# Kernel optimization log

Hardware: AMD Instinct MI355X
Metric: run time of the kernel (lower is better)

The kernel has to match this reference:

```python
import jax, jax.numpy as jnp
import numpy as np

IN, OUT, WS = 128, 64, 512
B, H, W = 4, 128, 128
GAIN = (2.0 / (1.0 + 0.2 ** 2)) ** 0.5  # util.lrelu_gain for leaky_relu(0.2)
EPS = 1e-8


def up2_bilinear_ac(x):
    # bilinear upsample x2, align_corners=True (torch F.upsample_bilinear semantics)
    _, _, h, w = x.shape
    ys = jnp.linspace(0.0, h - 1.0, 2 * h)
    xs = jnp.linspace(0.0, w - 1.0, 2 * w)
    y0 = jnp.floor(ys).astype(jnp.int32)
    y1 = jnp.minimum(y0 + 1, h - 1)
    wy = (ys - y0).astype(x.dtype)
    x0 = jnp.floor(xs).astype(jnp.int32)
    x1 = jnp.minimum(x0 + 1, w - 1)
    wx = (xs - x0).astype(x.dtype)
    t = x[:, :, y0, :] * (1 - wy)[None, None, :, None] + x[:, :, y1, :] * wy[None, None, :, None]
    return t[:, :, :, x0] * (1 - wx) + t[:, :, :, x1] * wx


def convt3(x, w):
    # torch conv_transpose2d(stride=1, padding=1, k=3) == conv2d with spatially
    # flipped kernel, weight layout [I,O,3,3] -> lax 'IOHW' spec, SAME padding.
    wf = w[:, :, ::-1, ::-1]
    return jax.lax.conv_general_dilated(
        x, wf, (1, 1), ((1, 1), (1, 1)),
        dimension_numbers=('NCHW', 'IOHW', 'NCHW'))


def mod_conv(x, style, w, he):
    # StyleGAN2 modulate + demodulate, expressed in fused activation form:
    # y[b,o] = demod[b,o] * convT(x[b] * style[b,:,None,None], he*W)  (same math
    # as building the per-sample grouped weight tensor in the original).
    wh = w * he                                  # [I,O,3,3]
    wsq = jnp.sum(wh * wh, axis=(2, 3))          # [I,O]
    d = jax.lax.rsqrt(jnp.einsum('bi,io->bo', style * style, wsq) + EPS)  # [B,O]
    y = convt3(x * style[:, :, None, None], wh)
    return y * d[:, :, None, None] * GAIN        # forward also multiplies by gain


def setup_inputs() -> dict:
    key = jax.random.key(0)
    ks = jax.random.split(key, 16)
    f = lambda k, s: jax.random.normal(k, s, dtype=jnp.float32)
    return {
        'x': f(ks[0], (B, IN, H, W)),
        'w': f(ks[1], (B, WS, 1, 1)),
        'conv1_w': f(ks[2], (IN, OUT, 3, 3)),
        'conv2_w': f(ks[3], (OUT, OUT, 3, 3)),
        'bias1': jnp.zeros((1, OUT, 1, 1), jnp.float32),
        'bias2': jnp.zeros((1, OUT, 1, 1), jnp.float32),
        'aaff1_w': f(ks[4], (IN, WS)),
        'aaff1_b': jnp.zeros((IN,), jnp.float32),
        'aaff2_w': f(ks[5], (OUT, WS)),
        'aaff2_b': jnp.zeros((OUT,), jnp.float32),
        'baff1_w': f(ks[6], (OUT,)) * 0.1,
        'baff2_w': f(ks[7], (OUT,)) * 0.1,
        'rgb_w': f(ks[8], (3, OUT)),
        'rgb_b': jnp.zeros((3,), jnp.float32),
        'noise1': f(ks[9], (B, 1, 2 * H, 2 * W)),
        'noise2': f(ks[10], (B, 1, 2 * H, 2 * W)),
    }


def reference(x, w, conv1_w, conv2_w, bias1, bias2, aaff1_w, aaff1_b,
              aaff2_w, aaff2_b, baff1_w, baff2_w, rgb_w, rgb_b,
              noise1, noise2):
    he1 = GAIN / (IN * 9) ** 0.5
    he2 = GAIN / (OUT * 9) ** 0.5
    he_a = 1.0 / WS ** 0.5
    he_rgb = 0.03 / OUT ** 0.5

    xu = up2_bilinear_ac(x)                       # [B,IN,2H,2W]
    wv = w[:, :, 0, 0]                            # [B,WS]

    s1 = jnp.einsum('ow,bw->bo', aaff1_w * he_a, wv) + aaff1_b
    h = mod_conv(xu, s1, conv1_w, he1)
    h = h + noise1 * baff1_w[None, :, None, None] + bias1
    h = jax.nn.leaky_relu(h, 0.2)

    s2 = jnp.einsum('ow,bw->bo', aaff2_w * he_a, wv) + aaff2_b
    h = mod_conv(h, s2, conv2_w, he2)
    h = h + noise2 * baff2_w[None, :, None, None] + bias2
    h = jax.nn.leaky_relu(h, 0.2)

    rgb = jnp.einsum('oc,bchw->bohw', rgb_w * he_rgb, h) + rgb_b[None, :, None, None]
    return (h, rgb)
```

## Files before the change

### kernel.cpp

```cpp
#include <hip/hip_runtime.h>
#include <hip/hip_bf16.h>
#include <math.h>

#define BN 4
#define CIN 128
#define COUT 64
#define WSDIM 512
#define HI 128
#define WI 128
#define HO 256
#define WO 256
#define EPSC 1e-8f
#define GAINC 1.3867504905630728f
#define HE1 (GAINC/33.941125496954285f)
#define HE2 (GAINC/24.0f)
#define SUP (127.0f/255.0f)

typedef __attribute__((ext_vector_type(8))) short s16x8;
typedef __attribute__((ext_vector_type(4))) float f32x4_t;
typedef __attribute__((ext_vector_type(4))) unsigned int u32x4;

static __device__ __forceinline__ float lrelu(float v){ return v > 0.f ? v : 0.2f*v; }
static __device__ __forceinline__ unsigned short bfbits(float v){
  __hip_bfloat16 h = __float2bfloat16(v);
  return *reinterpret_cast<unsigned short*>(&h);
}
static __device__ __forceinline__ unsigned int packbf(float a, float b){
  return (unsigned int)bfbits(a) | ((unsigned int)bfbits(b) << 16);
}
static __device__ __forceinline__ void gload_lds16(const void* g, void* l){
  __builtin_amdgcn_global_load_lds(
      (const __attribute__((address_space(1))) void*)g,
      (__attribute__((address_space(3))) void*)l, 16, 0, 0);
}

__global__ __launch_bounds__(256) void k_prep(
    const float* __restrict__ w, const float* __restrict__ c1w, const float* __restrict__ c2w,
    const float* __restrict__ a1w, const float* __restrict__ a1b,
    const float* __restrict__ a2w, const float* __restrict__ a2b,
    unsigned short* __restrict__ B1, unsigned short* __restrict__ B2,
    float* __restrict__ s1, float* __restrict__ s2,
    float* __restrict__ d1g, float* __restrict__ d2g,
    unsigned int* __restrict__ zpage)
{
  const int g = blockIdx.x, t = threadIdx.x;
  __shared__ float sh1[CIN];
  __shared__ float sh2[COUT];
  if (g < 144) {
    if (g == 0 && t < 64) zpage[t] = 0u;
    int cc = g / 36, r = g - cc * 36, k = r >> 2, ot = r & 3;
    for (int e = t; e < 512; e += 256) {
      int l = e >> 3, j = e & 7;
      int c = cc * 32 + (l >> 4) * 8 + j, o = ot * 16 + (l & 15);
      B1[g * 512 + e] = bfbits(c1w[(c * COUT + o) * 9 + (8 - k)] * HE1);
    }
  } else if (g < 288) {
    int g2 = g - 144;
    int cc = g2 / 36, r = g2 - cc * 36, k = r >> 2, ot = r & 3;
    for (int e = t; e < 512; e += 256) {
      int l = e >> 3, j = e & 7;
      int c = cc * 32 + (l >> 4) * 8 + j, o = ot * 16 + (l & 15);
      B2[g2 * 512 + e] = bfbits(c2w[(c * COUT + o) * 9 + (8 - k)] * HE2);
    }
  } else {
    const int b = g - 288;
    const float he_a = 0.044194173824159216f;
    const float* wv = w + b * WSDIM;
    if (t < CIN) {
      float acc = 0.f;
      const float* ap = a1w + t * WSDIM;
      for (int k = 0; k < WSDIM; ++k) acc += ap[k] * wv[k];
      float v = acc * he_a + a1b[t];
      sh1[t] = v; s1[b * CIN + t] = v;
    } else if (t < CIN + COUT) {
      int o = t - CIN;
      float acc = 0.f;
      const float* ap = a2w + o * WSDIM;
      for (int k = 0; k < WSDIM; ++k) acc += ap[k] * wv[k];
      float v = acc * he_a + a2b[o];
      sh2[o] = v; s2[b * COUT + o] = v;
    }
    __syncthreads();
    const int o = t >> 2, p = t & 3;
    float acc = 0.f;
    for (int c = p * 32; c < p * 32 + 32; ++c) {
      const float* wp = c1w + (size_t)(c * COUT + o) * 9;
      float ws_ = 0.f;
      #pragma unroll
      for (int k = 0; k < 9; ++k) ws_ += wp[k] * wp[k];
      acc += sh1[c] * sh1[c] * ws_;
    }
    acc += __shfl_xor(acc, 1); acc += __shfl_xor(acc, 2);
    if (p == 0) d1g[b * COUT + o] = rsqrtf(acc * HE1 * HE1 + EPSC) * GAINC;
    float ac2 = 0.f;
    for (int c = p * 16; c < p * 16 + 16; ++c) {
      const float* wp = c2w + (size_t)(c * COUT + o) * 9;
      float ws_ = 0.f;
      #pragma unroll
      for (int k = 0; k < 9; ++k) ws_ += wp[k] * wp[k];
      ac2 += sh2[c] * sh2[c] * ws_;
    }
    ac2 += __shfl_xor(ac2, 1); ac2 += __shfl_xor(ac2, 2);
    if (p == 0) d2g[b * COUT + o] = rsqrtf(ac2 * HE2 * HE2 + EPSC) * GAINC;
  }
}

__global__ __launch_bounds__(256) void k_conv1(
    const float* __restrict__ x, const unsigned short* __restrict__ B1pre,
    const float* __restrict__ s1, const float* __restrict__ noise1,
    const float* __restrict__ bias1, const float* __restrict__ baff1,
    const float* __restrict__ d1g, const float* __restrict__ s2,
    unsigned short* __restrict__ h1)
{
  const int id = blockIdx.x;
  const int swz = (id & 7) * 256 + (id >> 3);
  const int b = swz >> 9;
  const int oy0 = ((swz >> 4) & 31) * 8, ox0 = (swz & 15) * 16;
  const int tid = threadIdx.x;
  const int lane = tid & 63, wv = tid >> 6;
  const int lx = lane & 15, lg = lane >> 4;

  __shared__ __align__(16) float patch[3584];
  __shared__ __align__(16) unsigned int ldsA[180 * 16];
  __shared__ float s1L[CIN];

  const int ty = oy0 > 0 ? oy0 - 1 : 0;
  const int tx = ox0 > 0 ? ox0 - 1 : 0;
  const int py0 = min((ty * 127) / 255, HI - 7);
  const int px0 = min((tx * 127) / 255, WI - 12);
  const int px0a = px0 & ~3;

  if (tid < CIN) s1L[tid] = s1[b * CIN + tid];

  f32x4_t acc[2][4];
  #pragma unroll
  for (int i = 0; i < 2; ++i)
    #pragma unroll
    for (int j = 0; j < 4; ++j) acc[i][j] = (f32x4_t){0.f, 0.f, 0.f, 0.f};

  auto STAGE = [&](int cc) {
    const float* xb = x + (((size_t)b * CIN + cc * 32) << 14);
    #pragma unroll
    for (int i = 0; i < 3; ++i) {
      int ub = i * 256 + (wv << 6);
      int u = ub + lane;
      int p_ = u / 28, rem = u - p_ * 28;
      int ch = ((p_ & 3) << 3) | (p_ >> 2);
      int rr = rem >> 2, ck = rem & 3;
      int col = min(px0a + ck * 4, 124);
      const float* src = xb + ((size_t)ch << 14) + (py0 + rr) * WI + col;
      gload_lds16((const void*)src, (void*)&patch[(size_t)ub * 4]);
    }
    if (wv < 2) {
      int ub = 768 + (wv << 6);
      int u = ub + lane;
      int p_ = u / 28, rem = u - p_ * 28;
      int ch = ((p_ & 3) << 3) | (p_ >> 2);
      int rr = rem >> 2, ck = rem & 3;
      int col = min(px0a + ck * 4, 124);
      const float* src = xb + ((size_t)ch << 14) + (py0 + rr) * WI + col;
      gload_lds16((const void*)src, (void*)&patch[(size_t)ub * 4]);
    }
  };

  const s16x8* Bb = (const s16x8*)B1pre;

  STAGE(0);
  __syncthreads();
  for (int cc = 0; cc < 4; ++cc) {
    for (int e = tid; e < 720; e += 256) {
      int pos = e >> 2, q = e & 3;
      int ys = pos / 18, xs = pos - ys * 18;
      int yy = oy0 - 1 + ys, xx = ox0 - 1 + xs;
      u32x4 outv = {0u, 0u, 0u, 0u};
      if (yy >= 0 && yy < HO && xx >= 0 && xx < WO) {
        float fy = yy * SUP; int y0 = (int)fy; float wy = fy - (float)y0;
        float fx = xx * SUP; int x0 = (int)fx; float wx = fx - (float)x0;
        int r0 = y0 - py0, r1 = min(y0 + 1, HI - 1) - py0;
        int c0 = x0 - px0a;
        float v[8];
        #pragma unroll
        for (int j = 0; j < 8; ++j) {
          const float* pc = &patch[(j * 4 + q) * 112];
          float tl = pc[r0 * 16 + c0], tr = pc[r0 * 16 + c0 + 1];
          float bl = pc[r1 * 16 + c0], br = pc[r1 * 16 + c0 + 1];
          float t0 = tl + (bl - tl) * wy;
          float t1 = tr + (br - tr) * wy;
          v[j] = (t0 + (t1 - t0) * wx) * s1L[cc * 32 + q * 8 + j];
        }
        outv = (u32x4){packbf(v[0], v[1]), packbf(v[2], v[3]),
                       packbf(v[4], v[5]), packbf(v[6], v[7])};
      }
      *(u32x4*)(ldsA + pos * 16 + q * 4) = outv;
    }
    __syncthreads();
    if (cc < 3) STAGE(cc + 1);
    #pragma unroll
    for (int k = 0; k < 9; ++k) {
      const int dy = k / 3, dx = k - 3 * (k / 3);
      s16x8 b0 = Bb[((cc * 9 + k) * 4 + 0) * 64 + lane];
      s16x8 b1 = Bb[((cc * 9 + k) * 4 + 1) * 64 + lane];
      s16x8 b2 = Bb[((cc * 9 + k) * 4 + 2) * 64 + lane];
      s16x8 b3 = Bb[((cc * 9 + k) * 4 + 3) * 64 + lane];
      #pragma unroll
      for (int yi = 0; yi < 2; ++yi) {
        int row = (wv * 2 + yi + dy) * 18 + (lx + dx);
        s16x8 a = *(const s16x8*)((const char*)ldsA + (size_t)row * 64 + lg * 16);
        acc[yi][0] = __builtin_amdgcn_mfma_f32_16x16x32_bf16(a, b0, acc[yi][0], 0, 0, 0);
        acc[yi][1] = __builtin_amdgcn_mfma_f32_16x16x32_bf16(a, b1, acc[yi][1], 0, 0, 0);
        acc[yi][2] = __builtin_amdgcn_mfma_f32_16x16x32_bf16(a, b2, acc[yi][2], 0, 0, 0);
        acc[yi][3] = __builtin_amdgcn_mfma_f32_16x16x32_bf16(a, b3, acc[yi][3], 0, 0, 0);
      }
    }
    if (cc < 3) __syncthreads();
  }
  #pragma unroll
  for (int yi = 0; yi < 2; ++yi) {
    int y = oy0 + wv * 2 + yi;
    f32x4_t nv = *(const f32x4_t*)(noise1 + (size_t)b * HO * WO + (size_t)y * WO + ox0 + lg * 4);
    #pragma unroll
    for (int ot = 0; ot < 4; ++ot) {
      int o = ot * 16 + lx;
      float d = d1g[b * COUT + o], ba = baff1[o], bi = bias1[o], sv = s2[b * COUT + o];
      #pragma unroll
      for (int jj = 0; jj < 4; ++jj) {
        float v = acc[yi][ot][jj] * d + nv[jj] * ba + bi;
        v = lrelu(v) * sv;
        int xg = ox0 + lg * 4 + jj;
        h1[(((size_t)b * HO + y) * WO + xg) * COUT + o] = bfbits(v);
      }
    }
  }
}

__global__ __launch_bounds__(256) void k_conv2(
    const unsigned short* __restrict__ h1, const unsigned short* __restrict__ B2pre,
    const float* __restrict__ noise2, const float* __restrict__ bias2, const float* __restrict__ baff2,
    const float* __restrict__ d2g, const float* __restrict__ rgbw, const float* __restrict__ rgbb,
    const unsigned int* __restrict__ zpage,
    float* __restrict__ hout, float* __restrict__ rgbout)
{
  const int id = blockIdx.x;
  const int swz = (id & 7) * 128 + (id >> 3);
  const int b = swz >> 8;
  const int oy0 = ((swz >> 4) & 15) * 16, ox0 = (swz & 15) * 16;
  const int tid = threadIdx.x;
  const int lane = tid & 63, wv = tid >> 6;
  const int lx = lane & 15, lg = lane >> 4;

  __shared__ __align__(16) unsigned int ldsA[2][1536 * 4];

  f32x4_t acc[4][4];
  #pragma unroll
  for (int i = 0; i < 4; ++i)
    #pragma unroll
    for (int j = 0; j < 4; ++j) acc[i][j] = (f32x4_t){0.f, 0.f, 0.f, 0.f};

  const s16x8* Bb = (const s16x8*)B2pre;

  const int e0u = __builtin_amdgcn_readfirstlane(tid & ~63);
  #pragma unroll
  for (int cc = 0; cc < 2; ++cc) {
    #pragma unroll
    for (int i = 0; i < 6; ++i) {
      int ebase = i * 256 + e0u;
      int e = ebase + lane;
      int pos = e >> 2, q = e & 3;
      int ys = pos / 18, xs = pos - ys * 18;
      int yy = oy0 - 1 + ys, xx = ox0 - 1 + xs;
      bool ok = (e < 1296) && (yy >= 0) && (yy < HO) && (xx >= 0) && (xx < WO);
      const void* src = ok
          ? (const void*)(h1 + ((((size_t)b * HO + yy) * WO + xx) * COUT) + cc * 32 + q * 8)
          : (const void*)zpage;
      gload_lds16(src, (void*)&ldsA[cc][(size_t)ebase * 4]);
    }
  }
  __syncthreads();

  #pragma unroll
  for (int cc = 0; cc < 2; ++cc) {
    const char* bufc = (const char*)ldsA[cc];
    #pragma unroll
    for (int k = 0; k < 9; ++k) {
      const int dy = k / 3, dx = k - 3 * (k / 3);
      s16x8 b0 = Bb[((cc * 9 + k) * 4 + 0) * 64 + lane];
      s16x8 b1 = Bb[((cc * 9 + k) * 4 + 1) * 64 + lane];
      s16x8 b2 = Bb[((cc * 9 + k) * 4 + 2) * 64 + lane];
      s16x8 b3 = Bb[((cc * 9 + k) * 4 + 3) * 64 + lane];
      #pragma unroll
      for (int yi = 0; yi < 4; ++yi) {
        int row = (wv * 4 + yi + dy) * 18 + (lx + dx);
        s16x8 a = *(const s16x8*)(bufc + (size_t)row * 64 + lg * 16);
        acc[yi][0] = __builtin_amdgcn_mfma_f32_16x16x32_bf16(a, b0, acc[yi][0], 0, 0, 0);
        acc[yi][1] = __builtin_amdgcn_mfma_f32_16x16x32_bf16(a, b1, acc[yi][1], 0, 0, 0);
        acc[yi][2] = __builtin_amdgcn_mfma_f32_16x16x32_bf16(a, b2, acc[yi][2], 0, 0, 0);
        acc[yi][3] = __builtin_amdgcn_mfma_f32_16x16x32_bf16(a, b3, acc[yi][3], 0, 0, 0);
      }
    }
  }
  const float her = 0.03f / 8.0f;
  #pragma unroll
  for (int yi = 0; yi < 4; ++yi) {
    int y = oy0 + wv * 4 + yi;
    f32x4_t nv = *(const f32x4_t*)(noise2 + (size_t)b * HO * WO + (size_t)y * WO + ox0 + lg * 4);
    float r[3][4];
    #pragma unroll
    for (int ch = 0; ch < 3; ++ch)
      #pragma unroll
      for (int jj = 0; jj < 4; ++jj) r[ch][jj] = 0.f;
    #pragma unroll
    for (int ot = 0; ot < 4; ++ot) {
      int o = ot * 16 + lx;
      float d = d2g[b * COUT + o], ba = baff2[o], bi = bias2[o];
      float w0 = rgbw[o], w1 = rgbw[COUT + o], w2 = rgbw[2 * COUT + o];
      f32x4_t hv;
      #pragma unroll
      for (int jj = 0; jj < 4; ++jj) {
        float v = acc[yi][ot][jj] * d + nv[jj] * ba + bi;
        v = lrelu(v);
        hv[jj] = v;
        r[0][jj] += w0 * v; r[1][jj] += w1 * v; r[2][jj] += w2 * v;
      }
      *(f32x4_t*)(hout + ((size_t)(b * COUT + o) * HO + y) * WO + ox0 + lg * 4) = hv;
    }
    #pragma unroll
    for (int ch = 0; ch < 3; ++ch)
      #pragma unroll
      for (int jj = 0; jj < 4; ++jj) {
        float s = r[ch][jj];
        s += __shfl_xor(s, 1); s += __shfl_xor(s, 2);
        s += __shfl_xor(s, 4); s += __shfl_xor(s, 8);
        r[ch][jj] = s;
      }
    if (lx < 12) {
      float val = 0.f;
      #pragma unroll
      for (int ii = 0; ii < 12; ++ii) if (lx == ii) val = r[ii >> 2][ii & 3];
      int ch = lx >> 2, jj = lx & 3;
      rgbout[(((size_t)(b * 3 + ch)) * HO + y) * WO + ox0 + lg * 4 + jj] = val * her + rgbb[ch];
    }
  }
}

extern "C" void kernel_launch(void* const* d_in, const int* in_sizes, int n_in,
                              void* d_out, int out_size, void* d_ws, size_t ws_size,
                              hipStream_t stream) {
  const float* x      = (const float*)d_in[0];
  const float* w      = (const float*)d_in[1];
  const float* c1w    = (const float*)d_in[2];
  const float* c2w    = (const float*)d_in[3];
  const float* bias1  = (const float*)d_in[4];
  const float* bias2  = (const float*)d_in[5];
  const float* a1w    = (const float*)d_in[6];
  const float* a1b    = (const float*)d_in[7];
  const float* a2w    = (const float*)d_in[8];
  const float* a2b    = (const float*)d_in[9];
  const float* baff1  = (const float*)d_in[10];
  const float* baff2  = (const float*)d_in[11];
  const float* rgbw   = (const float*)d_in[12];
  const float* rgbb   = (const float*)d_in[13];
  const float* noise1 = (const float*)d_in[14];
  const float* noise2 = (const float*)d_in[15];

  const size_t h1_bytes = (size_t)BN * HO * WO * COUT * 2;
  unsigned short* h1 = (unsigned short*)d_ws;
  char* p = (char*)d_ws + h1_bytes;
  float* s1  = (float*)p;               p += BN * CIN * 4;
  float* s2  = (float*)p;               p += BN * COUT * 4;
  float* d1g = (float*)p;               p += BN * COUT * 4;
  float* d2g = (float*)p;               p += BN * COUT * 4;
  unsigned short* B1pre = (unsigned short*)p;  p += 144 * 512 * 2;
  unsigned short* B2pre = (unsigned short*)p;  p += 144 * 512 * 2;
  unsigned int* zpage = (unsigned int*)p;

  float* hout   = (float*)d_out;
  float* rgbout = hout + (size_t)BN * COUT * HO * WO;

  k_prep<<<292, 256, 0, stream>>>(w, c1w, c2w, a1w, a1b, a2w, a2b, B1pre, B2pre, s1, s2, d1g, d2g, zpage);
  k_conv1<<<2048, 256, 0, stream>>>(x, B1pre, s1, noise1, bias1, baff1, d1g, s2, h1);
  k_conv2<<<1024, 256, 0, stream>>>(h1, B2pre, noise2, bias2, baff2, d2g, rgbw, rgbb, zpage, hout, rgbout);
}
```

Baseline: 138.9 us.

## Pretranspose style-scaled input to channel-last bf16 before conv1

Adds a kernel that multiplies the input by the style vector, converts it to bf16 and transposes it to a channel-last layout. conv1 then stages the whole 7x13 pixel patch for all 128 channels once, instead of restaging an fp32 patch per 32-channel chunk. The bilinear gather reads 16-byte vectors of 8 packed channels and reuses precomputed interpolation indices. The cost is an extra kernel launch and an extra intermediate write and read of the input in global memory. The per-chunk prefetch overlap is removed, and the upsample input is now rounded to bf16 before interpolation rather than after.

```diff
diff --git a/kernel.cpp b/kernel.cpp
--- a/kernel.cpp
+++ b/kernel.cpp
@@ -105,10 +105,53 @@
   }
 }
 
+__global__ __launch_bounds__(256) void k_xt(
+    const float* __restrict__ x, const float* __restrict__ s1, unsigned short* __restrict__ XT)
+{
+  const int bid = blockIdx.x;
+  const int b = bid >> 7, y = bid & 127;
+  const int tid = threadIdx.x;
+  __shared__ float xs[32][133];
+  __shared__ float s1L[CIN];
+  if (tid < CIN) s1L[tid] = s1[b * CIN + tid];
+  const float* xb = x + (((size_t)b * CIN) << 14) + y * WI;
+  unsigned short* out = XT + (((size_t)(b * 128 + y)) << 7) * 128;
+
+  for (int chunk = 0; chunk < 4; ++chunk) {
+    __syncthreads();
+    {
+      int c = tid >> 3, x8 = (tid & 7) << 4;
+      const float* src = xb + (((size_t)(chunk * 32 + c)) << 14) + x8;
+      #pragma unroll
+      for (int k2 = 0; k2 < 4; ++k2) {
+        f32x4_t v = *(const f32x4_t*)(src + k2 * 4);
+        xs[c][x8 + k2 * 4 + 0] = v[0];
+        xs[c][x8 + k2 * 4 + 1] = v[1];
+        xs[c][x8 + k2 * 4 + 2] = v[2];
+        xs[c][x8 + k2 * 4 + 3] = v[3];
+      }
+    }
+    __syncthreads();
+    {
+      int xp = tid >> 1, half = tid & 1;
+      unsigned int pk[8];
+      #pragma unroll
+      for (int i2 = 0; i2 < 8; ++i2) {
+        int ch = half * 16 + i2 * 2;
+        float a  = xs[ch][xp]     * s1L[chunk * 32 + ch];
+        float bq = xs[ch + 1][xp] * s1L[chunk * 32 + ch + 1];
+        pk[i2] = packbf(a, bq);
+      }
+      unsigned short* dst = out + (size_t)xp * 128 + chunk * 32 + half * 16;
+      *(u32x4*)dst = *(u32x4*)pk;
+      *(u32x4*)(dst + 8) = *(u32x4*)(pk + 4);
+    }
+  }
+}
+
 __global__ __launch_bounds__(256) void k_conv1(
-    const float* __restrict__ x, const unsigned short* __restrict__ B1pre,
-    const float* __restrict__ s1, const float* __restrict__ noise1,
-    const float* __restrict__ bias1, const float* __restrict__ baff1,
+    const unsigned short* __restrict__ XT, const unsigned short* __restrict__ B1pre,
+    const float* __restrict__ noise1, const float* __restrict__ bias1, const float* __restrict__ baff1,
     const float* __restrict__ d1g, const float* __restrict__ s2,
     unsigned short* __restrict__ h1)
 {
@@ -120,81 +163,93 @@
   const int lane = tid & 63, wv = tid >> 6;
   const int lx = lane & 15, lg = lane >> 4;
 
-  __shared__ __align__(16) float patch[3584];
+  __shared__ __align__(16) unsigned int patch[1457 * 4];
   __shared__ __align__(16) unsigned int ldsA[180 * 16];
-  __shared__ float s1L[CIN];
 
   const int ty = oy0 > 0 ? oy0 - 1 : 0;
   const int tx = ox0 > 0 ? ox0 - 1 : 0;
   const int py0 = min((ty * 127) / 255, HI - 7);
-  const int px0 = min((tx * 127) / 255, WI - 12);
-  const int px0a = px0 & ~3;
-
-  if (tid < CIN) s1L[tid] = s1[b * CIN + tid];
-
-  f32x4_t acc[2][4];
-  #pragma unroll
-  for (int i = 0; i < 2; ++i)
-    #pragma unroll
-    for (int j = 0; j < 4; ++j) acc[i][j] = (f32x4_t){0.f, 0.f, 0.f, 0.f};
-
-  auto STAGE = [&](int cc) {
-    const float* xb = x + (((size_t)b * CIN + cc * 32) << 14);
-    #pragma unroll
-    for (int i = 0; i < 3; ++i) {
-      int ub = i * 256 + (wv << 6);
-      int u = ub + lane;
-      int p_ = u / 28, rem = u - p_ * 28;
-      int ch = ((p_ & 3) << 3) | (p_ >> 2);
-      int rr = rem >> 2, ck = rem & 3;
-      int col = min(px0a + ck * 4, 124);
-      const float* src = xb + ((size_t)ch << 14) + (py0 + rr) * WI + col;
-      gload_lds16((const void*)src, (void*)&patch[(size_t)ub * 4]);
-    }
-    if (wv < 2) {
-      int ub = 768 + (wv << 6);
-      int u = ub + lane;
-      int p_ = u / 28, rem = u - p_ * 28;
-      int ch = ((p_ & 3) << 3) | (p_ >> 2);
-      int rr = rem >> 2, ck = rem & 3;
-      int col = min(px0a + ck * 4, 124);
-      const float* src = xb + ((size_t)ch << 14) + (py0 + rr) * WI + col;
-      gload_lds16((const void*)src, (void*)&patch[(size_t)ub * 4]);
-    }
-  };
-
-  const s16x8* Bb = (const s16x8*)B1pre;
-
-  STAGE(0);
-  __syncthreads();
-  for (int cc = 0; cc < 4; ++cc) {
-    for (int e = tid; e < 720; e += 256) {
-      int pos = e >> 2, q = e & 3;
+  const int px0 = min((tx * 127) / 255, WI - 13);
+  const int q = tid & 3;
+
+  int a0[3], a1[3];
+  float gwy[3], gwx[3];
+  bool gok[3];
+  #pragma unroll
+  for (int i = 0; i < 3; ++i) {
+    int e = tid + i * 256;
+    gok[i] = false; a0[i] = 0; a1[i] = 0; gwy[i] = 0.f; gwx[i] = 0.f;
+    if (e < 720) {
+      int pos = e >> 2;
       int ys = pos / 18, xs = pos - ys * 18;
       int yy = oy0 - 1 + ys, xx = ox0 - 1 + xs;
-      u32x4 outv = {0u, 0u, 0u, 0u};
       if (yy >= 0 && yy < HO && xx >= 0 && xx < WO) {
-        float fy = yy * SUP; int y0 = (int)fy; float wy = fy - (float)y0;
-        float fx = xx * SUP; int x0 = (int)fx; float wx = fx - (float)x0;
+        gok[i] = true;
+        float fy = yy * SUP; int y0 = (int)fy; gwy[i] = fy - (float)y0;
+        float fx = xx * SUP; int x0 = (int)fx; gwx[i] = fx - (float)x0;
         int r0 = y0 - py0, r1 = min(y0 + 1, HI - 1) - py0;
-        int c0 = x0 - px0a;
-        float v[8];
-        #pragma unroll
-        for (int j = 0; j < 8; ++j) {
-          const float* pc = &patch[(j * 4 + q) * 112];
-          float tl = pc[r0 * 16 + c0], tr = pc[r0 * 16 + c0 + 1];
-          float bl = pc[r1 * 16 + c0], br = pc[r1 * 16 + c0 + 1];
-          float t0 = tl + (bl - tl) * wy;
-          float t1 = tr + (br - tr) * wy;
-          v[j] = (t0 + (t1 - t0) * wx) * s1L[cc * 32 + q * 8 + j];
+        int c0 = x0 - px0;
+        a0[i] = r0 * 13 + c0;
+        a1[i] = r1 * 13 + c0;
+      }
+    }
+  }
+
+  f32x4_t acc[2][4];
+  #pragma unroll
+  for (int i = 0; i < 2; ++i)
+    #pragma unroll
+    for (int j = 0; j < 4; ++j) acc[i][j] = (f32x4_t){0.f, 0.f, 0.f, 0.f};
+
+  if (tid == 0) { u32x4 z = {0u,0u,0u,0u}; *(u32x4*)(patch + (1456 << 2)) = z; }
+  #pragma unroll
+  for (int i = 0; i < 6; ++i) {
+    int u = tid + i * 256;
+    if (u < 1456) {
+      int g8 = u / 91, rem = u - g8 * 91;
+      int r = rem / 13, c = rem - r * 13;
+      const unsigned short* src = XT + ((((size_t)(b * 128 + py0 + r)) << 7) + (px0 + c)) * 128 + g8 * 8;
+      gload_lds16((const void*)src, (void*)(patch + ((size_t)u << 2)));
+    }
+  }
+  __syncthreads();
+
+  const s16x8* Bb = (const s16x8*)B1pre;
+  const u32x4* P = (const u32x4*)patch;
+
+  for (int cc = 0; cc < 4; ++cc) {
+    #pragma unroll
+    for (int i = 0; i < 3; ++i) {
+      int e = tid + i * 256;
+      if (e < 720) {
+        u32x4 outv = {0u, 0u, 0u, 0u};
+        if (gok[i]) {
+          int base = (cc * 4 + q) * 91;
+          u32x4 TL = P[base + a0[i]];
+          u32x4 TR = P[base + a0[i] + 1];
+          u32x4 BL = P[base + a1[i]];
+          u32x4 BR = P[base + a1[i] + 1];
+          float wy = gwy[i], wx = gwx[i];
+          #pragma unroll
+          for (int k2 = 0; k2 < 4; ++k2) {
+            float tl0 = __uint_as_float(TL[k2] << 16), tl1 = __uint_as_float(TL[k2] & 0xFFFF0000u);
+            float tr0 = __uint_as_float(TR[k2] << 16), tr1 = __uint_as_float(TR[k2] & 0xFFFF0000u);
+            float bl0 = __uint_as_float(BL[k2] << 16), bl1 = __uint_as_float(BL[k2] & 0xFFFF0000u);
+            float br0 = __uint_as_float(BR[k2] << 16), br1 = __uint_as_float(BR[k2] & 0xFFFF0000u);
+            float t0 = tl0 + (bl0 - tl0) * wy;
+            float t1 = tr0 + (br0 - tr0) * wy;
+            float v0 = t0 + (t1 - t0) * wx;
+            float u0 = tl1 + (bl1 - tl1) * wy;
+            float u1 = tr1 + (br1 - tr1) * wy;
+            float v1 = u0 + (u1 - u0) * wx;
+            outv[k2] = packbf(v0, v1);
+          }
         }
-        outv = (u32x4){packbf(v[0], v[1]), packbf(v[2], v[3]),
-                       packbf(v[4], v[5]), packbf(v[6], v[7])};
-      }
-      *(u32x4*)(ldsA + pos * 16 + q * 4) = outv;
+        int pos = (tid >> 2) + i * 64;
+        *(u32x4*)(ldsA + pos * 16 + q * 4) = outv;
+      }
     }
     __syncthreads();
-    if (cc < 3) STAGE(cc + 1);
     #pragma unroll
     for (int k = 0; k < 9; ++k) {
       const int dy = k / 3, dx = k - 3 * (k / 3);
@@ -371,12 +426,14 @@
   float* d2g = (float*)p;               p += BN * COUT * 4;
   unsigned short* B1pre = (unsigned short*)p;  p += 144 * 512 * 2;
   unsigned short* B2pre = (unsigned short*)p;  p += 144 * 512 * 2;
-  unsigned int* zpage = (unsigned int*)p;
+  unsigned int* zpage = (unsigned int*)p;      p += 256 * 4;
+  unsigned short* XT = (unsigned short*)p;
 
   float* hout   = (float*)d_out;
   float* rgbout = hout + (size_t)BN * COUT * HO * WO;
 
   k_prep<<<292, 256, 0, stream>>>(w, c1w, c2w, a1w, a1b, a2w, a2b, B1pre, B2pre, s1, s2, d1g, d2g, zpage);
-  k_conv1<<<2048, 256, 0, stream>>>(x, B1pre, s1, noise1, bias1, baff1, d1g, s2, h1);
+  k_xt<<<512, 256, 0, stream>>>(x, s1, XT);
+  k_conv1<<<2048, 256, 0, stream>>>(XT, B1pre, noise1, bias1, baff1, d1g, s2, h1);
   k_conv2<<<1024, 256, 0, stream>>>(h1, B2pre, noise2, bias2, baff2, d2g, rgbw, rgbb, zpage, hout, rgbout);
 }
```

Result: no change. 141.6 us (+2.0%).
